# Kernel tuning notes

Measured on AMD Instinct MI355X. Metric: run time of the kernel, lower is better.

## Reference

```python
import jax, jax.numpy as jnp
import numpy as np

B = 512      # number of ragged items
M = 256      # max item length (power of two)
D = 128      # EMBED_SIZE == dim
LEVELS = 8   # ceil(log2(M)) tree-reduction levels
EPS = 1e-5   # torch LayerNorm default


def _mlp(x, W1, b1, W2, b2, ln_w, ln_b):
    # Linear(2D->2D) -> ReLU -> Linear(2D->D) -> LayerNorm(D)
    h = jax.nn.relu(x @ W1 + b1)
    y = h @ W2 + b2
    mu = jnp.mean(y, axis=-1, keepdims=True)
    var = jnp.mean((y - mu) ** 2, axis=-1, keepdims=True)
    return (y - mu) * jax.lax.rsqrt(var + EPS) * ln_w + ln_b


def setup_inputs() -> dict:
    rng = np.random.default_rng(0)
    lengths = rng.integers(1, M + 1, size=B)
    limits = np.concatenate([[0], np.cumsum(lengths)]).astype(np.int64)
    T = int(limits[-1])
    ks = jax.random.split(jax.random.key(0), 5)
    s1 = 1.0 / np.sqrt(2 * D)  # torch Linear init bound, fan_in = 2*D
    s2 = 1.0 / np.sqrt(2 * D)
    return {
        "args": jax.random.normal(ks[0], (T, D), jnp.float32),
        "limits": jnp.asarray(limits),
        "W1": jax.random.uniform(ks[1], (2 * D, 2 * D), jnp.float32, -s1, s1),
        "b1": jax.random.uniform(ks[2], (2 * D,), jnp.float32, -s1, s1),
        "W2": jax.random.uniform(ks[3], (2 * D, D), jnp.float32, -s2, s2),
        "b2": jax.random.uniform(ks[4], (D,), jnp.float32, -s2, s2),
        "ln_w": jnp.ones((D,), jnp.float32),
        "ln_b": jnp.zeros((D,), jnp.float32),
    }


def reference(args, limits, W1, b1, W2, b2, ln_w, ln_b):
    lengths = jnp.diff(limits).astype(jnp.int32)  # [B]
    T = args.shape[0]
    # pad each ragged item to M and place it at the start of a 2M-1 tree buffer
    rows = limits[:-1, None].astype(jnp.int32) + jnp.arange(M, dtype=jnp.int32)[None, :]
    mask = jnp.arange(M)[None, :] < lengths[:, None]
    seq = jnp.where(mask[..., None], args[jnp.clip(rows, 0, T - 1)], 0.0)  # [B,M,D]
    buf0 = jnp.concatenate([seq, jnp.zeros((B, M - 1, D), seq.dtype)], axis=1)  # [B,2M-1,D]

    def reduce_item(buf, L):
        # level-synchronized binary tree reduction; odd leftover carries to next level
        s = jnp.int32(0)
        l = L
        for k in range(LEVELS):
            pmax = max(1, M >> (k + 1))  # static per-level pair capacity
            j = jnp.arange(pmax, dtype=jnp.int32)
            pairs = l // 2
            valid = j < pairs
            ia = jnp.where(valid, s + 2 * j, 0)
            a = buf[ia]          # [pmax, D]
            b = buf[ia + 1]      # [pmax, D]
            out = _mlp(jnp.concatenate([a, b], axis=-1), W1, b1, W2, b2, ln_w, ln_b)
            fill = jnp.where(valid, s + l + j, 2 * M - 1)  # OOB index -> dropped
            buf = buf.at[fill].set(out, mode="drop")
            s = s + 2 * pairs
            l = (l + 1) // 2
        return buf[2 * L - 2]  # root of the tree (== input element when L == 1)

    return jax.vmap(reduce_item)(buf0, lengths)  # [B, D]
```

## Files before the change

### kernel.cpp

```cpp
#include <hip/hip_runtime.h>
#include <stdint.h>

#define D 128

typedef __bf16 bf16x8 __attribute__((ext_vector_type(8)));
typedef float f32x4  __attribute__((ext_vector_type(4)));

__device__ __forceinline__ float b2f(ushort u) {
    uint x = ((uint)u) << 16;
    return __builtin_bit_cast(float, x);
}
__device__ __forceinline__ ushort f2b(float f) {
    uint u = __builtin_bit_cast(uint, f);
    u += 0x7FFFu + ((u >> 16) & 1u);
    return (ushort)(u >> 16);
}
__device__ __forceinline__ int swz(int b) { return b ^ (((b >> 9) & 7) << 4); }

__global__ void __launch_bounds__(512) prep_kernel(
    const float* __restrict__ W1, const float* __restrict__ W2,
    const int* __restrict__ limits,
    ushort* __restrict__ W1p, ushort* __restrict__ W2p,
    int4* __restrict__ chainTab)
{
    if (blockIdx.x < 192) {
        int g = blockIdx.x * 512 + threadIdx.x;
        if (g < 65536) {
            int t = g & 7, l = (g >> 3) & 63, nt = (g >> 9) & 15, kk = g >> 13;
            int krow = kk * 32 + (l >> 4) * 8 + t;
            int col  = nt * 16 + (l & 15);
            W1p[g] = f2b(W1[krow * 256 + col]);
        } else {
            int g2 = g - 65536;
            int t = g2 & 7, l = (g2 >> 3) & 63, nt = (g2 >> 9) & 7, kk = g2 >> 12;
            int krow = kk * 32 + (l >> 4) * 8 + t;
            int col  = nt * 16 + (l & 15);
            W2p[g2] = f2b(W2[krow * 128 + col]);
        }
        return;
    }
    __shared__ ushort Ls[512];
    __shared__ ushort rnkIdx[512];
    const int tid = threadIdx.x;
    int Lm = min(max(limits[tid + 1] - limits[tid], 1), 256);
    Ls[tid] = (ushort)Lm;
    __syncthreads();
    int rank = 0;
    for (int j = 0; j < 512; ++j) {
        int Lj = Ls[j];
        rank += (Lj > Lm) || (Lj == Lm && j < tid);
    }
    rnkIdx[rank] = (ushort)tid;
    __syncthreads();
    if (tid < 256) {
        int iA = rnkIdx[tid], iB = rnkIdx[511 - tid];
        int4 t;
        t.x = iA | (((int)Ls[iA]) << 16);
        t.y = iB | (((int)Ls[iB]) << 16);
        t.z = limits[iA];
        t.w = limits[iB];
        chainTab[tid] = t;
    }
}

template<int NMF>
__device__ __forceinline__ void level_body(
    char* __restrict__ Xw, const unsigned* __restrict__ sk,
    const uint4 (&w1r)[8][2], const uint4 (&w2r)[8],
    const float (&bb1)[2][4], const float (&bb2v)[4],
    const float (&lwv)[4], const float (&lbv)[4],
    float2* __restrict__ pbuf,
    const ushort* __restrict__ cpSk, const ushort* __restrict__ itOff,
    int G, bool doLeft, int tid, int lane, int w)
{
    constexpr int FPP   = (NMF >= 2) ? 2 : 1;
    constexpr int NPASS = NMF / FPP;

    #pragma unroll
    for (int p = 0; p < NPASS; ++p) {
        unsigned pa[FPP];
        #pragma unroll
        for (int mf = 0; mf < FPP; ++mf) pa[mf] = sk[(p * FPP + mf) * 16 + (lane & 15)];

        f32x4 acc1[2][FPP];
        #pragma unroll
        for (int n = 0; n < 2; ++n)
            #pragma unroll
            for (int mf = 0; mf < FPP; ++mf) acc1[n][mf] = f32x4{0.f, 0.f, 0.f, 0.f};

        #pragma unroll
        for (int kk = 0; kk < 8; ++kk) {
            uint4 xv[FPP];
            #pragma unroll
            for (int mf = 0; mf < FPP; ++mf) {
                int prow = (int)(pa[mf] & 0xFFFFu);
                xv[mf] = *(const uint4*)(Xw + (prow * 512 + ((kk * 64 + (lane >> 4) * 16) ^ ((prow & 7) << 4))));
            }
            #pragma unroll
            for (int n = 0; n < 2; ++n) {
                bf16x8 af = __builtin_bit_cast(bf16x8, w1r[kk][n]);
                #pragma unroll
                for (int mf = 0; mf < FPP; ++mf)
                    acc1[n][mf] = __builtin_amdgcn_mfma_f32_16x16x32_bf16(
                        af, __builtin_bit_cast(bf16x8, xv[mf]), acc1[n][mf], 0, 0, 0);
            }
        }
        __syncthreads();

        #pragma unroll
        for (int mf = 0; mf < FPP; ++mf) {
            if ((pa[mf] >> 16) != 0xFFFFu) {
                int prow = (int)(pa[mf] & 0xFFFFu);
                int rbase = prow * 512, sm = (prow & 7) << 4;
                #pragma unroll
                for (int n = 0; n < 2; ++n) {
                    float h0 = fmaxf(acc1[n][mf][0] + bb1[n][0], 0.f);
                    float h1 = fmaxf(acc1[n][mf][1] + bb1[n][1], 0.f);
                    float h2 = fmaxf(acc1[n][mf][2] + bb1[n][2], 0.f);
                    float h3 = fmaxf(acc1[n][mf][3] + bb1[n][3], 0.f);
                    uint2 pk;
                    pk.x = (uint)f2b(h0) | ((uint)f2b(h1) << 16);
                    pk.y = (uint)f2b(h2) | ((uint)f2b(h3) << 16);
                    *(uint2*)(Xw + (rbase + ((64 * w + 32 * n + 8 * (lane >> 4)) ^ sm))) = pk;
                }
            }
        }
    }
    __syncthreads();

    unsigned pa2[NMF];
    #pragma unroll
    for (int mf = 0; mf < NMF; ++mf) pa2[mf] = sk[mf * 16 + (lane & 15)];

    f32x4 acc2[NMF];
    #pragma unroll
    for (int mf = 0; mf < NMF; ++mf) acc2[mf] = f32x4{0.f, 0.f, 0.f, 0.f};

    #pragma unroll
    for (int kk = 0; kk < 8; ++kk) {
        bf16x8 af = __builtin_bit_cast(bf16x8, w2r[kk]);
        #pragma unroll
        for (int mf = 0; mf < NMF; ++mf) {
            int prow = (int)(pa2[mf] & 0xFFFFu);
            uint4 hv = *(const uint4*)(Xw + (prow * 512 + ((kk * 64 + (lane >> 4) * 16) ^ ((prow & 7) << 4))));
            acc2[mf] = __builtin_amdgcn_mfma_f32_16x16x32_bf16(
                af, __builtin_bit_cast(bf16x8, hv), acc2[mf], 0, 0, 0);
        }
    }

    #pragma unroll
    for (int mf = 0; mf < NMF; ++mf) {
        float s1 = 0.f, s2 = 0.f;
        #pragma unroll
        for (int i = 0; i < 4; ++i) {
            float v = acc2[mf][i] + bb2v[i];
            acc2[mf][i] = v; s1 += v; s2 += v * v;
        }
        s1 += __shfl_xor(s1, 16, 64); s2 += __shfl_xor(s2, 16, 64);
        s1 += __shfl_xor(s1, 32, 64); s2 += __shfl_xor(s2, 32, 64);
        if ((lane >> 4) == 0)
            pbuf[w * 128 + mf * 16 + (lane & 15)] = float2{s1, s2};
    }
    __syncthreads();

    #pragma unroll
    for (int mf = 0; mf < NMF; ++mf) {
        int yd = (int)(pa2[mf] >> 16);
        if (yd != 0xFFFF) {
            int p = mf * 16 + (lane & 15);
            float S1 = 0.f, S2 = 0.f;
            #pragma unroll
            for (int ww = 0; ww < 8; ++ww) {
                float2 o = pbuf[ww * 128 + p];
                S1 += o.x; S2 += o.y;
            }
            float mu = S1 * (1.f / 128.f);
            float var = S2 * (1.f / 128.f) - mu * mu;
            float rs = rsqrtf(var + 1e-5f);
            float v0 = (acc2[mf][0] - mu) * rs * lwv[0] + lbv[0];
            float v1 = (acc2[mf][1] - mu) * rs * lwv[1] + lbv[1];
            float v2 = (acc2[mf][2] - mu) * rs * lwv[2] + lbv[2];
            float v3 = (acc2[mf][3] - mu) * rs * lwv[3] + lbv[3];
            uint2 pk;
            pk.x = (uint)f2b(v0) | ((uint)f2b(v1) << 16);
            pk.y = (uint)f2b(v2) | ((uint)f2b(v3) << 16);
            *(uint2*)(Xw + swz(yd * 256 + (16 * w + 4 * (lane >> 4)) * 2)) = pk;
        }
    }
    if (doLeft) {
        #pragma unroll
        for (int q = 0; q < 2; ++q) {
            int it = q * 32 + (tid >> 4);
            if (it < G) {
                int srow = (int)cpSk[it];
                if (srow != 0xFFFF) {
                    int ch = tid & 15;
                    uint4 v = *(const uint4*)(Xw + swz(srow * 256 + ch * 16));
                    *(uint4*)(Xw + swz((int)itOff[it] * 256 + ch * 16)) = v;
                }
            }
        }
    }
}

__global__ void __launch_bounds__(512)
__attribute__((amdgpu_waves_per_eu(2, 2)))
tree_kernel(
    const float* __restrict__ args, const int4* __restrict__ chainTab,
    const ushort* __restrict__ W1p, const ushort* __restrict__ W2p,
    const float* __restrict__ b1, const float* __restrict__ b2,
    const float* __restrict__ lnw, const float* __restrict__ lnb,
    float* __restrict__ out)
{
    __shared__ __align__(16) char Xw[90112];
    __shared__ unsigned int schedAll[1536];
    __shared__ float2 pbuf[1024];
    __shared__ ushort cpSAll[8][2];
    __shared__ ushort itOff[2], itL[2], itOut[2];
    __shared__ int itRow[2];
    __shared__ int nPAll[8];

    const int tid = threadIdx.x, lane = tid & 63, w = tid >> 6;

    uint4 w1r[8][2];
    #pragma unroll
    for (int kk = 0; kk < 8; ++kk)
        #pragma unroll
        for (int n = 0; n < 2; ++n)
            w1r[kk][n] = *(const uint4*)(W1p + (size_t)(((kk * 16 + (w * 2 + n)) * 64 + lane) << 3));

    uint4 w2r[8];
    #pragma unroll
    for (int kk = 0; kk < 8; ++kk)
        w2r[kk] = *(const uint4*)(W2p + (size_t)(((kk * 8 + w) * 64 + lane) << 3));

    float bb1[2][4];
    #pragma unroll
    for (int n = 0; n < 2; ++n)
        #pragma unroll
        for (int i = 0; i < 4; ++i)
            bb1[n][i] = b1[32 * w + 16 * n + 4 * (lane >> 4) + i];
    float bb2v[4], lwv[4], lbv[4];
    #pragma unroll
    for (int i = 0; i < 4; ++i) {
        int c = 16 * w + 4 * (lane >> 4) + i;
        bb2v[i] = b2[c]; lwv[i] = lnw[c]; lbv[i] = lnb[c];
    }

    const int4 ct = chainTab[blockIdx.x];
    const int iA = ct.x & 0xFFFF, La = ct.x >> 16;
    const int iB = ct.y & 0xFFFF, Lb = ct.y >> 16;
    const int a0A = ct.z, a0B = ct.w;
    const int offBfull = (La + 1) & ~1;
    const bool split = (offBfull + Lb > 352);
    const int npass = split ? 2 : 1;

    for (int pass = 0; pass < npass; ++pass) {
        int G, L0, r0, o0, off1 = 0, L1 = 0, r1 = 0, o1 = 0;
        if (!split)          { G = 2; L0 = La; r0 = a0A; o0 = iA; off1 = offBfull; L1 = Lb; r1 = a0B; o1 = iB; }
        else if (pass == 0)  { G = 1; L0 = La; r0 = a0A; o0 = iA; }
        else                 { G = 1; L0 = Lb; r0 = a0B; o0 = iB; }

        __syncthreads();
        if (tid == 0) {
            itOff[0] = 0;            itL[0] = (ushort)L0; itRow[0] = r0; itOut[0] = (ushort)o0;
            itOff[1] = (ushort)off1; itL[1] = (ushort)L1; itRow[1] = r1; itOut[1] = (ushort)o1;
        }
        int nlev = (L0 > 1) ? (32 - __clz(L0 - 1)) : 0;
        if (G > 1 && L1 > 1) nlev = max(nlev, 32 - __clz(L1 - 1));

        if (w == 0) {
            int lA_ = L0, lB_ = (G > 1) ? L1 : 0;
            for (int k = 0; k < nlev; ++k) {
                int pA = lA_ >> 1, pB = lB_ >> 1, nPk = pA + pB;
                if (lane == 0) {
                    nPAll[k] = nPk;
                    cpSAll[k][0] = (lA_ > 1 && (lA_ & 1)) ? (ushort)(lA_ - 1) : (ushort)0xFFFF;
                    cpSAll[k][1] = (lB_ > 1 && (lB_ & 1)) ? (ushort)(off1 + lB_ - 1) : (ushort)0xFFFF;
                }
                #pragma unroll
                for (int rep = 0; rep < 3; ++rep) {
                    int e = lane + rep * 64;
                    unsigned entry = 0xFFFF0000u;
                    if (e < pA)
                        entry = (unsigned)e | ((unsigned)((lA_ & 1) + e) << 16);
                    else if (e < nPk) {
                        int j = e - pA;
                        entry = (unsigned)((off1 >> 1) + j) | ((unsigned)(off1 + (lB_ & 1) + j) << 16);
                    }
                    schedAll[k * 192 + e] = entry;
                }
                lA_ = pA + (lA_ & 1);
                lB_ = pB + (lB_ & 1);
            }
        } else {
            for (int job = tid - 64; job < 5632; job += 448) {
                int r = job >> 4, ch = job & 15;
                int src = -1;
                if (r < L0) src = r0 + r;
                else if (G > 1 && r >= off1 && r < off1 + L1) src = r1 + (r - off1);
                if (src >= 0) {
                    const float4 f0 = *(const float4*)(args + (size_t)src * D + ch * 8);
                    const float4 f1 = *(const float4*)(args + (size_t)src * D + ch * 8 + 4);
                    uint4 pk;
                    pk.x = (uint)f2b(f0.x) | ((uint)f2b(f0.y) << 16);
                    pk.y = (uint)f2b(f0.z) | ((uint)f2b(f0.w) << 16);
                    pk.z = (uint)f2b(f1.x) | ((uint)f2b(f1.y) << 16);
                    pk.w = (uint)f2b(f1.z) | ((uint)f2b(f1.w) << 16);
                    *(uint4*)(Xw + swz(r * 256 + ch * 16)) = pk;
                }
            }
        }
        __syncthreads();

        for (int k = 0; k < nlev; ++k) {
            const int nP = nPAll[k];
            if (nP == 0) break;
            int done = 0;
            while (done < nP) {
                const int chunk = min(nP - done, 128);
                const int nMf = (chunk + 15) >> 4;
                const bool last = (done + chunk >= nP);
                const unsigned* sk = schedAll + k * 192 + done;
                if (nMf > 4)
                    level_body<8>(Xw, sk, w1r, w2r, bb1, bb2v, lwv, lbv, pbuf, cpSAll[k], itOff, G, last, tid, lane, w);
                else if (nMf > 2)
                    level_body<4>(Xw, sk, w1r, w2r, bb1, bb2v, lwv, lbv, pbuf, cpSAll[k], itOff, G, last, tid, lane, w);
                else if (nMf == 2)
                    level_body<2>(Xw, sk, w1r, w2r, bb1, bb2v, lwv, lbv, pbuf, cpSAll[k], itOff, G, last, tid, lane, w);
                else
                    level_body<1>(Xw, sk, w1r, w2r, bb1, bb2v, lwv, lbv, pbuf, cpSAll[k], itOff, G, last, tid, lane, w);
                __syncthreads();
                done += chunk;
            }
        }

        for (int j = tid; j < G * 32; j += 512) {
            int it = j >> 5, grp = j & 31;
            float4 o;
            if ((int)itL[it] == 1) {
                o = *(const float4*)(args + (size_t)itRow[it] * D + grp * 4);
            } else {
                uint2 v = *(const uint2*)(Xw + swz((int)itOff[it] * 256 + grp * 8));
                o.x = b2f((ushort)(v.x & 0xFFFFu));
                o.y = b2f((ushort)(v.x >> 16));
                o.z = b2f((ushort)(v.y & 0xFFFFu));
                o.w = b2f((ushort)(v.y >> 16));
            }
            *(float4*)(out + (size_t)itOut[it] * D + grp * 4) = o;
        }
    }
}

extern "C" void kernel_launch(void* const* d_in, const int* in_sizes, int n_in,
                              void* d_out, int out_size, void* d_ws, size_t ws_size,
                              hipStream_t stream) {
    const float* args   = (const float*)d_in[0];
    const int*   limits = (const int*)d_in[1];
    const float* W1     = (const float*)d_in[2];
    const float* b1     = (const float*)d_in[3];
    const float* W2     = (const float*)d_in[4];
    const float* b2     = (const float*)d_in[5];
    const float* lnw    = (const float*)d_in[6];
    const float* lnb    = (const float*)d_in[7];

    char* ws = (char*)d_ws;
    ushort* W1p      = (ushort*)(ws);
    ushort* W2p      = (ushort*)(ws + 131072);
    int4*   chainTab = (int4*)  (ws + 196608);

    prep_kernel<<<193, 512, 0, stream>>>(W1, W2, limits, W1p, W2p, chainTab);
    tree_kernel<<<256, 512, 0, stream>>>(args, chainTab, W1p, W2p, b1, b2, lnw, lnb,
                                         (float*)d_out);
}
```

Baseline: 64.90 us.

## Process one ragged item per block instead of pairing two items per block

Each block now reduces a single item rather than a long/short pair, with the grid doubled to 512 blocks and items still dispatched in descending length order. Shared memory drops from about 90 KB to 64 KB and the wave-occupancy hint is relaxed from exactly 2 to at least 4 waves per EU, so more blocks can be resident per CU. The schedule, odd-element carry and output logic are simplified to match. The trade-off is that each block does less MFMA work per level and loads the register-resident weights twice as often across the grid, while long items no longer share their sync steps with a short partner.

```diff
diff --git a/kernel.cpp b/kernel.cpp
--- a/kernel.cpp
+++ b/kernel.cpp
@@ -21,7 +21,7 @@
     const float* __restrict__ W1, const float* __restrict__ W2,
     const int* __restrict__ limits,
     ushort* __restrict__ W1p, ushort* __restrict__ W2p,
-    int4* __restrict__ chainTab)
+    int2* __restrict__ itemTab)
 {
     if (blockIdx.x < 192) {
         int g = blockIdx.x * 512 + threadIdx.x;
@@ -54,12 +54,8 @@
     __syncthreads();
     if (tid < 256) {
         int iA = rnkIdx[tid], iB = rnkIdx[511 - tid];
-        int4 t;
-        t.x = iA | (((int)Ls[iA]) << 16);
-        t.y = iB | (((int)Ls[iB]) << 16);
-        t.z = limits[iA];
-        t.w = limits[iB];
-        chainTab[tid] = t;
+        itemTab[2 * tid]     = int2{ iA | (((int)Ls[iA]) << 16), limits[iA] };
+        itemTab[2 * tid + 1] = int2{ iB | (((int)Ls[iB]) << 16), limits[iB] };
     }
 }
 
@@ -69,9 +65,8 @@
     const uint4 (&w1r)[8][2], const uint4 (&w2r)[8],
     const float (&bb1)[2][4], const float (&bb2v)[4],
     const float (&lwv)[4], const float (&lbv)[4],
-    float2* __restrict__ pbuf,
-    const ushort* __restrict__ cpSk, const ushort* __restrict__ itOff,
-    int G, bool doLeft, int tid, int lane, int w)
+    float2* __restrict__ pbuf, int cpS,
+    int tid, int lane, int w)
 {
     constexpr int FPP   = (NMF >= 2) ? 2 : 1;
     constexpr int NPASS = NMF / FPP;
@@ -187,37 +182,25 @@
             *(uint2*)(Xw + swz(yd * 256 + (16 * w + 4 * (lane >> 4)) * 2)) = pk;
         }
     }
-    if (doLeft) {
-        #pragma unroll
-        for (int q = 0; q < 2; ++q) {
-            int it = q * 32 + (tid >> 4);
-            if (it < G) {
-                int srow = (int)cpSk[it];
-                if (srow != 0xFFFF) {
-                    int ch = tid & 15;
-                    uint4 v = *(const uint4*)(Xw + swz(srow * 256 + ch * 16));
-                    *(uint4*)(Xw + swz((int)itOff[it] * 256 + ch * 16)) = v;
-                }
-            }
-        }
+    if (cpS != 0xFFFF && tid < 16) {
+        uint4 v = *(const uint4*)(Xw + swz(cpS * 256 + tid * 16));
+        *(uint4*)(Xw + swz(tid * 16)) = v;
     }
 }
 
 __global__ void __launch_bounds__(512)
-__attribute__((amdgpu_waves_per_eu(2, 2)))
+__attribute__((amdgpu_waves_per_eu(4)))
 tree_kernel(
-    const float* __restrict__ args, const int4* __restrict__ chainTab,
+    const float* __restrict__ args, const int2* __restrict__ itemTab,
     const ushort* __restrict__ W1p, const ushort* __restrict__ W2p,
     const float* __restrict__ b1, const float* __restrict__ b2,
     const float* __restrict__ lnw, const float* __restrict__ lnb,
     float* __restrict__ out)
 {
-    __shared__ __align__(16) char Xw[90112];
-    __shared__ unsigned int schedAll[1536];
+    __shared__ __align__(16) char Xw[65536];
+    __shared__ unsigned int schedAll[1024];
     __shared__ float2 pbuf[1024];
-    __shared__ ushort cpSAll[8][2];
-    __shared__ ushort itOff[2], itL[2], itOut[2];
-    __shared__ int itRow[2];
+    __shared__ int cpSAll[8];
     __shared__ int nPAll[8];
 
     const int tid = threadIdx.x, lane = tid & 63, w = tid >> 6;
@@ -247,108 +230,77 @@
         bb2v[i] = b2[c]; lwv[i] = lnw[c]; lbv[i] = lnb[c];
     }
 
-    const int4 ct = chainTab[blockIdx.x];
-    const int iA = ct.x & 0xFFFF, La = ct.x >> 16;
-    const int iB = ct.y & 0xFFFF, Lb = ct.y >> 16;
-    const int a0A = ct.z, a0B = ct.w;
-    const int offBfull = (La + 1) & ~1;
-    const bool split = (offBfull + Lb > 352);
-    const int npass = split ? 2 : 1;
-
-    for (int pass = 0; pass < npass; ++pass) {
-        int G, L0, r0, o0, off1 = 0, L1 = 0, r1 = 0, o1 = 0;
-        if (!split)          { G = 2; L0 = La; r0 = a0A; o0 = iA; off1 = offBfull; L1 = Lb; r1 = a0B; o1 = iB; }
-        else if (pass == 0)  { G = 1; L0 = La; r0 = a0A; o0 = iA; }
-        else                 { G = 1; L0 = Lb; r0 = a0B; o0 = iB; }
-
+    const int2 it2 = itemTab[blockIdx.x];
+    const int iOut = it2.x & 0xFFFF;
+    const int L0   = it2.x >> 16;
+    const int r0   = it2.y;
+    const int nlev = (L0 > 1) ? (32 - __clz(L0 - 1)) : 0;
+
+    if (w == 0) {
+        int l = L0;
+        for (int k = 0; k < nlev; ++k) {
+            int pA = l >> 1;
+            if (lane == 0) {
+                nPAll[k]  = pA;
+                cpSAll[k] = (l > 1 && (l & 1)) ? (l - 1) : 0xFFFF;
+            }
+            #pragma unroll
+            for (int rep = 0; rep < 2; ++rep) {
+                int e = lane + rep * 64;
+                unsigned entry = (e < pA)
+                    ? ((unsigned)e | ((unsigned)((l & 1) + e) << 16))
+                    : 0xFFFF0000u;
+                schedAll[k * 128 + e] = entry;
+            }
+            l = pA + (l & 1);
+        }
+    } else {
+        const int njob = L0 * 16;
+        for (int job = tid - 64; job < njob; job += 448) {
+            int r = job >> 4, ch = job & 15;
+            int src = r0 + r;
+            const float4 f0 = *(const float4*)(args + (size_t)src * D + ch * 8);
+            const float4 f1 = *(const float4*)(args + (size_t)src * D + ch * 8 + 4);
+            uint4 pk;
+            pk.x = (uint)f2b(f0.x) | ((uint)f2b(f0.y) << 16);
+            pk.y = (uint)f2b(f0.z) | ((uint)f2b(f0.w) << 16);
+            pk.z = (uint)f2b(f1.x) | ((uint)f2b(f1.y) << 16);
+            pk.w = (uint)f2b(f1.z) | ((uint)f2b(f1.w) << 16);
+            *(uint4*)(Xw + swz(r * 256 + ch * 16)) = pk;
+        }
+    }
+    __syncthreads();
+
+    for (int k = 0; k < nlev; ++k) {
+        const int nP = nPAll[k];
+        if (nP == 0) break;
+        const int nMf = (nP + 15) >> 4;
+        const unsigned* sk = schedAll + k * 128;
+        const int cpS = cpSAll[k];
+        if (nMf > 4)
+            level_body<8>(Xw, sk, w1r, w2r, bb1, bb2v, lwv, lbv, pbuf, cpS, tid, lane, w);
+        else if (nMf > 2)
+            level_body<4>(Xw, sk, w1r, w2r, bb1, bb2v, lwv, lbv, pbuf, cpS, tid, lane, w);
+        else if (nMf == 2)
+            level_body<2>(Xw, sk, w1r, w2r, bb1, bb2v, lwv, lbv, pbuf, cpS, tid, lane, w);
+        else
+            level_body<1>(Xw, sk, w1r, w2r, bb1, bb2v, lwv, lbv, pbuf, cpS, tid, lane, w);
         __syncthreads();
-        if (tid == 0) {
-            itOff[0] = 0;            itL[0] = (ushort)L0; itRow[0] = r0; itOut[0] = (ushort)o0;
-            itOff[1] = (ushort)off1; itL[1] = (ushort)L1; itRow[1] = r1; itOut[1] = (ushort)o1;
-        }
-        int nlev = (L0 > 1) ? (32 - __clz(L0 - 1)) : 0;
-        if (G > 1 && L1 > 1) nlev = max(nlev, 32 - __clz(L1 - 1));
-
-        if (w == 0) {
-            int lA_ = L0, lB_ = (G > 1) ? L1 : 0;
-            for (int k = 0; k < nlev; ++k) {
-                int pA = lA_ >> 1, pB = lB_ >> 1, nPk = pA + pB;
-                if (lane == 0) {
-                    nPAll[k] = nPk;
-                    cpSAll[k][0] = (lA_ > 1 && (lA_ & 1)) ? (ushort)(lA_ - 1) : (ushort)0xFFFF;
-                    cpSAll[k][1] = (lB_ > 1 && (lB_ & 1)) ? (ushort)(off1 + lB_ - 1) : (ushort)0xFFFF;
-                }
-                #pragma unroll
-                for (int rep = 0; rep < 3; ++rep) {
-                    int e = lane + rep * 64;
-                    unsigned entry = 0xFFFF0000u;
-                    if (e < pA)
-                        entry = (unsigned)e | ((unsigned)((lA_ & 1) + e) << 16);
-                    else if (e < nPk) {
-                        int j = e - pA;
-                        entry = (unsigned)((off1 >> 1) + j) | ((unsigned)(off1 + (lB_ & 1) + j) << 16);
-                    }
-                    schedAll[k * 192 + e] = entry;
-                }
-                lA_ = pA + (lA_ & 1);
-                lB_ = pB + (lB_ & 1);
-            }
+    }
+
+    if (tid < 32) {
+        int grp = tid;
+        float4 o;
+        if (L0 == 1) {
+            o = *(const float4*)(args + (size_t)r0 * D + grp * 4);
         } else {
-            for (int job = tid - 64; job < 5632; job += 448) {
-                int r = job >> 4, ch = job & 15;
-                int src = -1;
-                if (r < L0) src = r0 + r;
-                else if (G > 1 && r >= off1 && r < off1 + L1) src = r1 + (r - off1);
-                if (src >= 0) {
-                    const float4 f0 = *(const float4*)(args + (size_t)src * D + ch * 8);
-                    const float4 f1 = *(const float4*)(args + (size_t)src * D + ch * 8 + 4);
-                    uint4 pk;
-                    pk.x = (uint)f2b(f0.x) | ((uint)f2b(f0.y) << 16);
-                    pk.y = (uint)f2b(f0.z) | ((uint)f2b(f0.w) << 16);
-                    pk.z = (uint)f2b(f1.x) | ((uint)f2b(f1.y) << 16);
-                    pk.w = (uint)f2b(f1.z) | ((uint)f2b(f1.w) << 16);
-                    *(uint4*)(Xw + swz(r * 256 + ch * 16)) = pk;
-                }
-            }
-        }
-        __syncthreads();
-
-        for (int k = 0; k < nlev; ++k) {
-            const int nP = nPAll[k];
-            if (nP == 0) break;
-            int done = 0;
-            while (done < nP) {
-                const int chunk = min(nP - done, 128);
-                const int nMf = (chunk + 15) >> 4;
-                const bool last = (done + chunk >= nP);
-                const unsigned* sk = schedAll + k * 192 + done;
-                if (nMf > 4)
-                    level_body<8>(Xw, sk, w1r, w2r, bb1, bb2v, lwv, lbv, pbuf, cpSAll[k], itOff, G, last, tid, lane, w);
-                else if (nMf > 2)
-                    level_body<4>(Xw, sk, w1r, w2r, bb1, bb2v, lwv, lbv, pbuf, cpSAll[k], itOff, G, last, tid, lane, w);
-                else if (nMf == 2)
-                    level_body<2>(Xw, sk, w1r, w2r, bb1, bb2v, lwv, lbv, pbuf, cpSAll[k], itOff, G, last, tid, lane, w);
-                else
-                    level_body<1>(Xw, sk, w1r, w2r, bb1, bb2v, lwv, lbv, pbuf, cpSAll[k], itOff, G, last, tid, lane, w);
-                __syncthreads();
-                done += chunk;
-            }
-        }
-
-        for (int j = tid; j < G * 32; j += 512) {
-            int it = j >> 5, grp = j & 31;
-            float4 o;
-            if ((int)itL[it] == 1) {
-                o = *(const float4*)(args + (size_t)itRow[it] * D + grp * 4);
-            } else {
-                uint2 v = *(const uint2*)(Xw + swz((int)itOff[it] * 256 + grp * 8));
-                o.x = b2f((ushort)(v.x & 0xFFFFu));
-                o.y = b2f((ushort)(v.x >> 16));
-                o.z = b2f((ushort)(v.y & 0xFFFFu));
-                o.w = b2f((ushort)(v.y >> 16));
-            }
-            *(float4*)(out + (size_t)itOut[it] * D + grp * 4) = o;
-        }
+            uint2 v = *(const uint2*)(Xw + swz(grp * 8));
+            o.x = b2f((ushort)(v.x & 0xFFFFu));
+            o.y = b2f((ushort)(v.x >> 16));
+            o.z = b2f((ushort)(v.y & 0xFFFFu));
+            o.w = b2f((ushort)(v.y >> 16));
+        }
+        *(float4*)(out + (size_t)iOut * D + grp * 4) = o;
     }
 }
 
@@ -365,11 +317,11 @@
     const float* lnb    = (const float*)d_in[7];
 
     char* ws = (char*)d_ws;
-    ushort* W1p      = (ushort*)(ws);
-    ushort* W2p      = (ushort*)(ws + 131072);
-    int4*   chainTab = (int4*)  (ws + 196608);
-
-    prep_kernel<<<193, 512, 0, stream>>>(W1, W2, limits, W1p, W2p, chainTab);
-    tree_kernel<<<256, 512, 0, stream>>>(args, chainTab, W1p, W2p, b1, b2, lnw, lnb,
+    ushort* W1p     = (ushort*)(ws);
+    ushort* W2p     = (ushort*)(ws + 131072);
+    int2*   itemTab = (int2*)  (ws + 196608);
+
+    prep_kernel<<<193, 512, 0, stream>>>(W1, W2, limits, W1p, W2p, itemTab);
+    tree_kernel<<<512, 512, 0, stream>>>(args, itemTab, W1p, W2p, b1, b2, lnw, lnb,
                                          (float*)d_out);
 }
```

New measurement: 180.8 us. 179% more time.

## Fuse prep kernel into tree kernel and widen per-pass M-fragment batching

Applied to the files above, without the earlier changes.

Removes the separate prep launch. Each tree block now loads the fp32 weights, converts them to bf16 and packs its own register fragments. Each block also recomputes the length ranking from limits to find its pair of items. This avoids a kernel launch and the workspace round trip, at the cost of every block doing a redundant 512x512 rank loop and strided fp32 weight reads. It also raises the MFMA fragments processed per pass from 2 to 4, which increases register pressure.

```diff
diff --git a/kernel.cpp b/kernel.cpp
--- a/kernel.cpp
+++ b/kernel.cpp
@@ -16,52 +16,6 @@
     return (ushort)(u >> 16);
 }
 __device__ __forceinline__ int swz(int b) { return b ^ (((b >> 9) & 7) << 4); }
-
-__global__ void __launch_bounds__(512) prep_kernel(
-    const float* __restrict__ W1, const float* __restrict__ W2,
-    const int* __restrict__ limits,
-    ushort* __restrict__ W1p, ushort* __restrict__ W2p,
-    int4* __restrict__ chainTab)
-{
-    if (blockIdx.x < 192) {
-        int g = blockIdx.x * 512 + threadIdx.x;
-        if (g < 65536) {
-            int t = g & 7, l = (g >> 3) & 63, nt = (g >> 9) & 15, kk = g >> 13;
-            int krow = kk * 32 + (l >> 4) * 8 + t;
-            int col  = nt * 16 + (l & 15);
-            W1p[g] = f2b(W1[krow * 256 + col]);
-        } else {
-            int g2 = g - 65536;
-            int t = g2 & 7, l = (g2 >> 3) & 63, nt = (g2 >> 9) & 7, kk = g2 >> 12;
-            int krow = kk * 32 + (l >> 4) * 8 + t;
-            int col  = nt * 16 + (l & 15);
-            W2p[g2] = f2b(W2[krow * 128 + col]);
-        }
-        return;
-    }
-    __shared__ ushort Ls[512];
-    __shared__ ushort rnkIdx[512];
-    const int tid = threadIdx.x;
-    int Lm = min(max(limits[tid + 1] - limits[tid], 1), 256);
-    Ls[tid] = (ushort)Lm;
-    __syncthreads();
-    int rank = 0;
-    for (int j = 0; j < 512; ++j) {
-        int Lj = Ls[j];
-        rank += (Lj > Lm) || (Lj == Lm && j < tid);
-    }
-    rnkIdx[rank] = (ushort)tid;
-    __syncthreads();
-    if (tid < 256) {
-        int iA = rnkIdx[tid], iB = rnkIdx[511 - tid];
-        int4 t;
-        t.x = iA | (((int)Ls[iA]) << 16);
-        t.y = iB | (((int)Ls[iB]) << 16);
-        t.z = limits[iA];
-        t.w = limits[iB];
-        chainTab[tid] = t;
-    }
-}
 
 template<int NMF>
 __device__ __forceinline__ void level_body(
@@ -73,7 +27,7 @@
     const ushort* __restrict__ cpSk, const ushort* __restrict__ itOff,
     int G, bool doLeft, int tid, int lane, int w)
 {
-    constexpr int FPP   = (NMF >= 2) ? 2 : 1;
+    constexpr int FPP   = (NMF >= 4) ? 4 : NMF;
     constexpr int NPASS = NMF / FPP;
 
     #pragma unroll
@@ -206,8 +160,8 @@
 __global__ void __launch_bounds__(512)
 __attribute__((amdgpu_waves_per_eu(2, 2)))
 tree_kernel(
-    const float* __restrict__ args, const int4* __restrict__ chainTab,
-    const ushort* __restrict__ W1p, const ushort* __restrict__ W2p,
+    const float* __restrict__ args, const int* __restrict__ limits,
+    const float* __restrict__ W1, const float* __restrict__ W2,
     const float* __restrict__ b1, const float* __restrict__ b2,
     const float* __restrict__ lnw, const float* __restrict__ lnb,
     float* __restrict__ out)
@@ -215,6 +169,8 @@
     __shared__ __align__(16) char Xw[90112];
     __shared__ unsigned int schedAll[1536];
     __shared__ float2 pbuf[1024];
+    __shared__ ushort Ls[512];
+    __shared__ int plan[4];
     __shared__ ushort cpSAll[8][2];
     __shared__ ushort itOff[2], itL[2], itOut[2];
     __shared__ int itRow[2];
@@ -226,13 +182,29 @@
     #pragma unroll
     for (int kk = 0; kk < 8; ++kk)
         #pragma unroll
-        for (int n = 0; n < 2; ++n)
-            w1r[kk][n] = *(const uint4*)(W1p + (size_t)(((kk * 16 + (w * 2 + n)) * 64 + lane) << 3));
+        for (int n = 0; n < 2; ++n) {
+            const float* src = W1 + (size_t)(kk * 32 + (lane >> 4) * 8) * 256 + (w * 2 + n) * 16 + (lane & 15);
+            uint r[4];
+            #pragma unroll
+            for (int h = 0; h < 4; ++h) {
+                float a = src[(2 * h) * 256], bb = src[(2 * h + 1) * 256];
+                r[h] = (uint)f2b(a) | ((uint)f2b(bb) << 16);
+            }
+            w1r[kk][n] = uint4{r[0], r[1], r[2], r[3]};
+        }
 
     uint4 w2r[8];
     #pragma unroll
-    for (int kk = 0; kk < 8; ++kk)
-        w2r[kk] = *(const uint4*)(W2p + (size_t)(((kk * 8 + w) * 64 + lane) << 3));
+    for (int kk = 0; kk < 8; ++kk) {
+        const float* src = W2 + (size_t)(kk * 32 + (lane >> 4) * 8) * 128 + w * 16 + (lane & 15);
+        uint r[4];
+        #pragma unroll
+        for (int h = 0; h < 4; ++h) {
+            float a = src[(2 * h) * 128], bb = src[(2 * h + 1) * 128];
+            r[h] = (uint)f2b(a) | ((uint)f2b(bb) << 16);
+        }
+        w2r[kk] = uint4{r[0], r[1], r[2], r[3]};
+    }
 
     float bb1[2][4];
     #pragma unroll
@@ -247,10 +219,23 @@
         bb2v[i] = b2[c]; lwv[i] = lnw[c]; lbv[i] = lnb[c];
     }
 
-    const int4 ct = chainTab[blockIdx.x];
-    const int iA = ct.x & 0xFFFF, La = ct.x >> 16;
-    const int iB = ct.y & 0xFFFF, Lb = ct.y >> 16;
-    const int a0A = ct.z, a0B = ct.w;
+    {
+        int lim0 = limits[tid], lim1 = limits[tid + 1];
+        int Lm = min(max(lim1 - lim0, 1), 256);
+        Ls[tid] = (ushort)Lm;
+        __syncthreads();
+        int rank = 0;
+        for (int j = 0; j < 512; ++j) {
+            int Lj = Ls[j];
+            rank += (Lj > Lm) || (Lj == Lm && j < tid);
+        }
+        if (rank == (int)blockIdx.x)       { plan[0] = tid | (Lm << 16); plan[2] = lim0; }
+        if (rank == 511 - (int)blockIdx.x) { plan[1] = tid | (Lm << 16); plan[3] = lim0; }
+        __syncthreads();
+    }
+    const int iA = plan[0] & 0xFFFF, La = plan[0] >> 16;
+    const int iB = plan[1] & 0xFFFF, Lb = plan[1] >> 16;
+    const int a0A = plan[2], a0B = plan[3];
     const int offBfull = (La + 1) & ~1;
     const bool split = (offBfull + Lb > 352);
     const int npass = split ? 2 : 1;
@@ -364,12 +349,6 @@
     const float* lnw    = (const float*)d_in[6];
     const float* lnb    = (const float*)d_in[7];
 
-    char* ws = (char*)d_ws;
-    ushort* W1p      = (ushort*)(ws);
-    ushort* W2p      = (ushort*)(ws + 131072);
-    int4*   chainTab = (int4*)  (ws + 196608);
-
-    prep_kernel<<<193, 512, 0, stream>>>(W1, W2, limits, W1p, W2p, chainTab);
-    tree_kernel<<<256, 512, 0, stream>>>(args, chainTab, W1p, W2p, b1, b2, lnw, lnb,
+    tree_kernel<<<256, 512, 0, stream>>>(args, limits, W1, W2, b1, b2, lnw, lnb,
                                          (float*)d_out);
 }
```

New measurement: 66.70 us. 2.8% more time.
